# Optimization experiments

Measured on AMD Instinct MI355X. Metric: run time of the kernel, lower is better.

## Reference

```python
import jax, jax.numpy as jnp
import numpy as np

B, T, I, H, O = 256, 256, 16, 256, 11
HYP_HID = 512
BLD = 8
N1 = H * I + H * H + 2 * H        # RNN cell params (W_ih, W_hh, b_ih, b_hh)
N2 = O * H + O                    # readout params (W_out, b_out)


def setup_inputs() -> dict:
    key = jax.random.key(0)
    k = jax.random.split(key, 4)
    bld = jax.random.normal(k[0], (B, BLD), dtype=jnp.float32)
    stimulus = jax.random.normal(k[1], (B, T, I), dtype=jnp.float32)
    # hypnet MLP: bld -> relu -> flat per-sample params; small init to keep tanh unsaturated
    W1 = jax.random.normal(k[2], (BLD, HYP_HID), dtype=jnp.float32) * 0.05
    b1 = jnp.zeros((HYP_HID,), dtype=jnp.float32)
    W2 = jax.random.normal(k[3], (HYP_HID, N1 + N2), dtype=jnp.float32) * 0.02
    b2 = jnp.zeros((N1 + N2,), dtype=jnp.float32)
    return {"bld": bld, "stimulus": stimulus, "W1": W1, "b1": b1, "W2": W2, "b2": b2}


def reference(bld, stimulus, W1, b1, W2, b2):
    # hypernetwork: per-sample flat params [B, N1+N2]
    flat = jax.nn.relu(bld @ W1 + b1) @ W2 + b2
    params1, params2 = flat[:, :N1], flat[:, N1:]

    # unpack per-sample RNN cell params
    o = 0
    W_ih = params1[:, o:o + H * I].reshape(B, H, I); o += H * I
    W_hh = params1[:, o:o + H * H].reshape(B, H, H); o += H * H
    b_ih = params1[:, o:o + H]; o += H
    b_hh = params1[:, o:o + H]
    W_out = params2[:, :O * H].reshape(B, O, H)
    b_out = params2[:, O * H:].reshape(B, O)

    # shift stimulus right by one step with a zero frame (teacher forcing input)
    rnn_input = jnp.concatenate(
        [jnp.zeros((B, 1, I), dtype=stimulus.dtype), stimulus[:, :-1]], axis=1)

    # precompute input projection for all steps: [B, T, H]
    x_proj = jnp.einsum('bti,bhi->bth', rnn_input, W_ih) + b_ih[:, None, :]

    def step(h, xp_t):  # h: [B, H], xp_t: [B, H]
        h_next = jnp.tanh(xp_t + jnp.einsum('bh,bgh->bg', h, W_hh) + b_hh)
        return h_next, h_next

    h0 = jnp.zeros((B, H), dtype=stimulus.dtype)
    h_last, out_tm = jax.lax.scan(step, h0, jnp.swapaxes(x_proj, 0, 1))
    output1 = jnp.swapaxes(out_tm, 0, 1)  # [B, T, H]

    # per-sample linear readout [B, T, O]
    output2 = jnp.einsum('bth,boh->bto', output1, W_out) + b_out[:, None, :]
    output2 = jnp.nan_to_num(output2, nan=0.0)

    output_act = jax.nn.sigmoid(output2[:, :, :3])
    output_bldi = output2[:, :, 3:]
    h = h_last[None]  # [1, B, H]
    return (output_act, output_bldi, h, params1, params2)
```

## Files before the change

kernel.cpp:

```cpp
#include <hip/hip_runtime.h>

typedef unsigned short u16;
typedef unsigned int u32;
using short8   = __attribute__((ext_vector_type(8))) short;
using floatx4  = __attribute__((ext_vector_type(4))) float;
using half_t   = _Float16;
using half2_t  = __attribute__((ext_vector_type(2))) _Float16;
using halfx8   = __attribute__((ext_vector_type(8))) _Float16;

constexpr int B_ = 256, T_ = 256, I_ = 16, H_ = 256, O_ = 11;
constexpr int HYP = 512;
constexpr int N1_ = H_ * I_ + H_ * H_ + 2 * H_;
constexpr int N2_ = O_ * H_ + O_;
constexpr int GN  = N1_ + N2_;

constexpr size_t OUT_ACT  = 0;
constexpr size_t OUT_BLDI = (size_t)B_ * T_ * 3;
constexpr size_t OUT_H    = OUT_BLDI + (size_t)B_ * T_ * 8;
constexpr size_t OUT_P1   = OUT_H + (size_t)B_ * H_;
constexpr size_t OUT_P2   = OUT_P1 + (size_t)B_ * N1_;

__device__ inline void bar_lds() {
    asm volatile("s_waitcnt lgkmcnt(0)\n\ts_barrier" ::: "memory");
}

__device__ inline float bf2f(u16 u) {
    union { u32 i; float f; } v; v.i = ((u32)u) << 16; return v.f;
}
__device__ inline u16 f2bf(float f) {
    u32 x = __float_as_uint(f);
    u32 r = (x + 0x7fffu + ((x >> 16) & 1u)) >> 16;
    return (u16)r;
}

__device__ inline bool sniff_f32(const void* p) {
    const u16* w = (const u16*)p;
    const int lane = threadIdx.x & 63;
    u16 u = w[lane * 2];
    unsigned e = (u >> 7) & 0xFF;
    bool inband = (u == 0) || (e >= 77 && e <= 140);
    return __popcll(__ballot(inband)) < 56;
}

__device__ inline float ldr(const void* p, size_t i, bool f32) {
    return f32 ? ((const float*)p)[i] : bf2f(((const u16*)p)[i]);
}

__global__ void h1_kernel(const void* __restrict__ bld, const void* __restrict__ W1,
                          const void* __restrict__ b1, u16* __restrict__ h1) {
    const bool bldf = sniff_f32(bld);
    const bool w1f  = sniff_f32(W1);
    const bool b1f  = sniff_f32(b1);
    const int b = blockIdx.x;
    const int j = threadIdx.x;
    float acc = ldr(b1, j, b1f);
#pragma unroll
    for (int k = 0; k < 8; k++)
        acc += ldr(bld, b * 8 + k, bldf) * ldr(W1, k * HYP + j, w1f);
    h1[b * HYP + j] = f2bf(fmaxf(acc, 0.f));
}

constexpr int KS_ = 32;
constexpr int NST = HYP / KS_;
constexpr int TKP = 40;

template<bool W2F32>
__device__ void gemm_body(const u16* __restrict__ A, const void* __restrict__ Bm,
                          const void* __restrict__ b2, bool b2f,
                          float* __restrict__ out) {
    __shared__ alignas(16) u16 tileT[2][64][TKP];

    const int nb   = blockIdx.x * 64;
    const int tid  = threadIdx.x;
    const int lane = tid & 63;
    const int wid  = tid >> 6;
    const int l15  = lane & 15;
    const int q    = lane >> 4;

    int  col[4]; bool cv[4];
#pragma unroll
    for (int j = 0; j < 4; j++) {
        int c = nb + j * 16 + l15;
        cv[j]  = (c < GN);
        col[j] = cv[j] ? c : (GN - 1);
    }

    const u16* ap[4];
#pragma unroll
    for (int i = 0; i < 4; i++)
        ap[i] = A + (wid * 64 + i * 16 + l15) * HYP + q * 8;

    const int scol_i = tid & 63;
    const int kq     = tid >> 6;
    int gc = nb + scol_i;
    if (gc >= GN) gc = GN - 1;
    const size_t colOff = (size_t)gc;

    float pfw[8]; u16 pbw[8];
    short8 afc[4];

    {
        float t0[8]; u16 t1[8];
#pragma unroll
        for (int e = 0; e < 8; e++) {
            const size_t ro = (size_t)(kq * 8 + e) * (size_t)GN + colOff;
            if constexpr (W2F32) t0[e] = ((const float*)Bm)[ro];
            else                 t1[e] = ((const u16*)Bm)[ro];
        }
        short8 wv8;
#pragma unroll
        for (int e = 0; e < 8; e++) {
            if constexpr (W2F32) wv8[e] = (short)f2bf(t0[e]);
            else                 wv8[e] = (short)t1[e];
        }
        *(short8*)&tileT[0][scol_i][kq * 8] = wv8;
    }
#pragma unroll
    for (int e = 0; e < 8; e++) {
        const size_t ro = (size_t)(KS_ + kq * 8 + e) * (size_t)GN + colOff;
        if constexpr (W2F32) pfw[e] = ((const float*)Bm)[ro];
        else                 pbw[e] = ((const u16*)Bm)[ro];
    }
#pragma unroll
    for (int i = 0; i < 4; i++) afc[i] = *(const short8*)(ap[i]);
    bar_lds();

    floatx4 acc[4][4] = {};

#pragma unroll
    for (int ks = 0; ks < NST; ks++) {
        const int cur = ks & 1;

        short8 bfr[4];
#pragma unroll
        for (int j = 0; j < 4; j++)
            bfr[j] = *(const short8*)&tileT[cur][j * 16 + l15][q * 8];

        short8 afn[4];
        if (ks + 1 < NST) {
#pragma unroll
            for (int i = 0; i < 4; i++)
                afn[i] = *(const short8*)(ap[i] + (ks + 1) * KS_);
        }
        float pfn[8]; u16 pbn[8];
        if (ks + 2 < NST) {
#pragma unroll
            for (int e = 0; e < 8; e++) {
                const size_t ro = (size_t)((ks + 2) * KS_ + kq * 8 + e) * (size_t)GN + colOff;
                if constexpr (W2F32) pfn[e] = ((const float*)Bm)[ro];
                else                 pbn[e] = ((const u16*)Bm)[ro];
            }
        }
        if (ks + 1 < NST) {
            short8 wv8;
#pragma unroll
            for (int e = 0; e < 8; e++) {
                if constexpr (W2F32) wv8[e] = (short)f2bf(pfw[e]);
                else                 wv8[e] = (short)pbw[e];
            }
            *(short8*)&tileT[cur ^ 1][scol_i][kq * 8] = wv8;
        }

#pragma unroll
        for (int i = 0; i < 4; i++)
#pragma unroll
            for (int j = 0; j < 4; j++)
                acc[i][j] = __builtin_amdgcn_mfma_f32_16x16x32_bf16(afc[i], bfr[j], acc[i][j], 0, 0, 0);
        bar_lds();

#pragma unroll
        for (int i = 0; i < 4; i++) afc[i] = afn[i];
#pragma unroll
        for (int e = 0; e < 8; e++) {
            if constexpr (W2F32) pfw[e] = pfn[e];
            else                 pbw[e] = pbn[e];
        }
    }

    const bool isP2 = (nb >= N1_);
#pragma unroll
    for (int j = 0; j < 4; j++) {
        const float bias = ldr(b2, col[j], b2f);
#pragma unroll
        for (int i = 0; i < 4; i++) {
            const int mbase = wid * 64 + i * 16 + q * 4;
#pragma unroll
            for (int r = 0; r < 4; r++) {
                if (cv[j]) {
                    const float v = acc[i][j][r] + bias;
                    const int m = mbase + r;
                    size_t dst;
                    if (isP2) dst = OUT_P2 + (size_t)m * N2_ + (size_t)(col[j] - N1_);
                    else      dst = OUT_P1 + (size_t)m * N1_ + (size_t)col[j];
                    out[dst] = v;
                }
            }
        }
    }
}
__global__ __launch_bounds__(256) void gemm_kernel(const u16* A, const void* Bm,
                                                   const void* b2, float* out) {
    const bool w2f = sniff_f32(Bm);
    const bool b2f = sniff_f32(b2);
    if (w2f) gemm_body<true>(A, Bm, b2, b2f, out);
    else     gemm_body<false>(A, Bm, b2, b2f, out);
}

constexpr int HROW = 256;
constexpr int XROW = 40;

__global__ __launch_bounds__(512, 1) void rnn_kernel(const void* __restrict__ stim,
                                                     float* __restrict__ out) {
    const bool stf = sniff_f32(stim);
    const int b    = blockIdx.x;
    const int tid  = threadIdx.x;
    const int lane = tid & 63;
    const int wv   = tid >> 6;
    const int l15  = lane & 15;
    const int q    = lane >> 4;

    const float* p1 = out + OUT_P1 + (size_t)b * N1_;
    const float* p2 = out + OUT_P2 + (size_t)b * N2_;

    __shared__ alignas(16) half_t hist[(T_ + 1) * HROW];
    __shared__ alignas(16) half_t stim_s[T_ * XROW];

    if (stf) {
        const float2* sp = (const float2*)stim + (size_t)b * T_ * 8;
        for (int idx = tid; idx < (T_ - 1) * 8; idx += 512) {
            const int tt = idx >> 3, pr = idx & 7;
            float2 v = sp[idx];
            half2_t h; h.x = (half_t)v.x; h.y = (half_t)v.y;
            *(half2_t*)&stim_s[(tt + 1) * XROW + pr * 2] = h;
        }
    } else {
        const u32* sp = (const u32*)((const u16*)stim + (size_t)b * T_ * I_);
        for (int idx = tid; idx < (T_ - 1) * 8; idx += 512) {
            const int tt = idx >> 3, pr = idx & 7;
            u32 u = sp[idx];
            union { u32 i; float f; } lo2, hi2;
            lo2.i = u << 16; hi2.i = u & 0xffff0000u;
            half2_t h; h.x = (half_t)lo2.f; h.y = (half_t)hi2.f;
            *(half2_t*)&stim_s[(tt + 1) * XROW + pr * 2] = h;
        }
    }
    {
        u32* ss = (u32*)stim_s;
        if (tid < 256) {
            const int base = tid * (XROW / 2);
            ss[base + 8] = 0x00003C00u;
#pragma unroll
            for (int z = 9; z < XROW / 2; z++) ss[base + z] = 0u;
        }
        if (tid < 8)   ss[tid] = 0u;
        if (tid < 128) ((u32*)hist)[tid] = 0u;
    }

    halfx8 Wf[2][9];
    {
        const float* WH  = p1 + H_ * I_;
        const float* BIH = p1 + H_ * I_ + H_ * H_;
#pragma unroll
        for (int it = 0; it < 2; it++) {
            const int rr = 32 * wv + it * 16 + l15;
#pragma unroll
            for (int kt = 0; kt < 8; kt++) {
                const float4* wp = (const float4*)(WH + (size_t)rr * H_ + kt * 32 + q * 8);
                float4 r0 = wp[0], r1 = wp[1];
                halfx8 f;
                f[0] = (half_t)r0.x; f[1] = (half_t)r0.y; f[2] = (half_t)r0.z; f[3] = (half_t)r0.w;
                f[4] = (half_t)r1.x; f[5] = (half_t)r1.y; f[6] = (half_t)r1.z; f[7] = (half_t)r1.w;
                Wf[it][kt] = f;
            }
            halfx8 fx;
#pragma unroll
            for (int j = 0; j < 8; j++) fx[j] = (half_t)0.f;
            if (q < 2) {
                const float4* ip = (const float4*)(p1 + (size_t)rr * I_ + q * 8);
                float4 r0 = ip[0], r1 = ip[1];
                fx[0] = (half_t)r0.x; fx[1] = (half_t)r0.y; fx[2] = (half_t)r0.z; fx[3] = (half_t)r0.w;
                fx[4] = (half_t)r1.x; fx[5] = (half_t)r1.y; fx[6] = (half_t)r1.z; fx[7] = (half_t)r1.w;
            } else if (q == 2) {
                fx[0] = (half_t)(BIH[rr] + BIH[H_ + rr]);
            }
            Wf[it][8] = fx;
        }
    }
    __syncthreads();

    for (int t = 0; t < T_; t++) {
        halfx8 af[9];
        const half_t* hr = hist + (size_t)t * HROW + q * 8;
#pragma unroll
        for (int kt = 0; kt < 8; kt++)
            af[kt] = *(const halfx8*)(hr + kt * 32);
        af[8] = *(const halfx8*)(stim_s + (size_t)t * XROW + q * 8);

        floatx4 acc[2] = {};
#pragma unroll
        for (int kt = 0; kt < 9; kt++) {
            acc[0] = __builtin_amdgcn_mfma_f32_16x16x32_f16(af[kt], Wf[0][kt], acc[0], 0, 0, 0);
            acc[1] = __builtin_amdgcn_mfma_f32_16x16x32_f16(af[kt], Wf[1][kt], acc[1], 0, 0, 0);
        }

        half_t* hw = hist + (size_t)(t + 1) * HROW;
#pragma unroll
        for (int it = 0; it < 2; it++) {
            const float s  = acc[it][0];
            const float e  = __expf(2.f * s);
            const float hn = 1.f - 2.f / (e + 1.f);
            if (lane < 16) {
                hw[32 * wv + it * 16 + l15] = (half_t)hn;
                if (t == T_ - 1) out[OUT_H + (size_t)b * H_ + 32 * wv + it * 16 + l15] = hn;
            }
        }
        bar_lds();
    }

    halfx8 Wo[8];
    float bo = 0.f;
    {
#pragma unroll
        for (int kt = 0; kt < 8; kt++) {
            halfx8 f;
#pragma unroll
            for (int j = 0; j < 8; j++) f[j] = (half_t)0.f;
            if (l15 < O_) {
                const float* wp = p2 + (size_t)l15 * H_ + kt * 32 + q * 8;
#pragma unroll
                for (int j = 0; j < 8; j++) f[j] = (half_t)wp[j];
            }
            Wo[kt] = f;
        }
        if (l15 < O_) bo = p2[O_ * H_ + l15];
    }

#pragma unroll
    for (int m = 0; m < 2; m++) {
        const int tb = (2 * wv + m) * 16;
        const half_t* hr = hist + (size_t)(tb + l15 + 1) * HROW + q * 8;
        floatx4 acc = {};
#pragma unroll
        for (int kt = 0; kt < 8; kt++) {
            halfx8 a = *(const halfx8*)(hr + kt * 32);
            acc = __builtin_amdgcn_mfma_f32_16x16x32_f16(a, Wo[kt], acc, 0, 0, 0);
        }
        if (l15 < O_) {
            const int o = l15;
#pragma unroll
            for (int r = 0; r < 4; r++) {
                const int tt = tb + q * 4 + r;
                float v2 = acc[r] + bo;
                if (o < 3) out[OUT_ACT + (size_t)b * T_ * 3 + (size_t)tt * 3 + o] = 1.f / (1.f + __expf(-v2));
                else       out[OUT_BLDI + (size_t)b * T_ * 8 + (size_t)tt * 8 + (o - 3)] = v2;
            }
        }
    }
}

extern "C" void kernel_launch(void* const* d_in, const int* in_sizes, int n_in,
                              void* d_out, int out_size, void* d_ws, size_t ws_size,
                              hipStream_t stream) {
    (void)in_sizes; (void)n_in; (void)out_size; (void)d_ws; (void)ws_size;
    const void* bld  = d_in[0];
    const void* stim = d_in[1];
    const void* W1   = d_in[2];
    const void* b1   = d_in[3];
    const void* W2   = d_in[4];
    const void* b2   = d_in[5];
    float* out = (float*)d_out;
    u16* h1 = (u16*)out;

    h1_kernel<<<B_, HYP, 0, stream>>>(bld, W1, b1, h1);
    gemm_kernel<<<(GN + 63) / 64, 256, 0, stream>>>(h1, W2, b2, out);
    rnn_kernel<<<B_, 512, 0, stream>>>(stim, out);
}
```

Baseline: 437.7 us.

## Precompute input projection for all timesteps before the recurrent loop

Before the time loop, the input projection plus the combined biases is computed for all 256 steps with MFMAs and stored in the hidden-history buffer. That slot is read back each step and overwritten with the new hidden state. This removes one MFMA pair and one LDS load per serial step. The tanh epilogue is also spread across 32 lanes instead of 16 running two passes, and MFMA issue priority is raised with s_setprio. The cost is an extra fp16 rounding of the input projection and an upfront pass over all timesteps.

```diff
diff --git a/kernel.cpp b/kernel.cpp
--- a/kernel.cpp
+++ b/kernel.cpp
@@ -256,7 +256,8 @@
         if (tid < 128) ((u32*)hist)[tid] = 0u;
     }
 
-    halfx8 Wf[2][9];
+    halfx8 Wf[2][8];
+    halfx8 Wx[2];
     {
         const float* WH  = p1 + H_ * I_;
         const float* BIH = p1 + H_ * I_ + H_ * H_;
@@ -283,36 +284,49 @@
             } else if (q == 2) {
                 fx[0] = (half_t)(BIH[rr] + BIH[H_ + rr]);
             }
-            Wf[it][8] = fx;
+            Wx[it] = fx;
         }
     }
     __syncthreads();
 
+#pragma unroll
+    for (int tm = 0; tm < 16; tm++) {
+        halfx8 ax = *(const halfx8*)(stim_s + (size_t)(16 * tm + l15) * XROW + q * 8);
+        floatx4 xa0 = __builtin_amdgcn_mfma_f32_16x16x32_f16(ax, Wx[0], floatx4{}, 0, 0, 0);
+        floatx4 xa1 = __builtin_amdgcn_mfma_f32_16x16x32_f16(ax, Wx[1], floatx4{}, 0, 0, 0);
+#pragma unroll
+        for (int r = 0; r < 4; r++) {
+            const int trow = 16 * tm + 4 * q + r;
+            hist[(size_t)(trow + 1) * HROW + 32 * wv + l15]      = (half_t)xa0[r];
+            hist[(size_t)(trow + 1) * HROW + 32 * wv + 16 + l15] = (half_t)xa1[r];
+        }
+    }
+    __syncthreads();
+
+    const int g32 = 32 * wv + (lane & 31);
     for (int t = 0; t < T_; t++) {
-        halfx8 af[9];
+        halfx8 af[8];
         const half_t* hr = hist + (size_t)t * HROW + q * 8;
 #pragma unroll
         for (int kt = 0; kt < 8; kt++)
             af[kt] = *(const halfx8*)(hr + kt * 32);
-        af[8] = *(const halfx8*)(stim_s + (size_t)t * XROW + q * 8);
-
-        floatx4 acc[2] = {};
-#pragma unroll
-        for (int kt = 0; kt < 9; kt++) {
-            acc[0] = __builtin_amdgcn_mfma_f32_16x16x32_f16(af[kt], Wf[0][kt], acc[0], 0, 0, 0);
-            acc[1] = __builtin_amdgcn_mfma_f32_16x16x32_f16(af[kt], Wf[1][kt], acc[1], 0, 0, 0);
-        }
-
-        half_t* hw = hist + (size_t)(t + 1) * HROW;
-#pragma unroll
-        for (int it = 0; it < 2; it++) {
-            const float s  = acc[it][0];
+        const float xp = (float)hist[(size_t)(t + 1) * HROW + g32];
+
+        floatx4 acc0 = {}, acc1 = {};
+        __builtin_amdgcn_s_setprio(1);
+#pragma unroll
+        for (int kt = 0; kt < 8; kt++) {
+            acc0 = __builtin_amdgcn_mfma_f32_16x16x32_f16(af[kt], Wf[0][kt], acc0, 0, 0, 0);
+            acc1 = __builtin_amdgcn_mfma_f32_16x16x32_f16(af[kt], Wf[1][kt], acc1, 0, 0, 0);
+        }
+        __builtin_amdgcn_s_setprio(0);
+
+        if (lane < 32) {
+            const float s  = ((lane < 16) ? acc0[0] : acc1[0]) + xp;
             const float e  = __expf(2.f * s);
             const float hn = 1.f - 2.f / (e + 1.f);
-            if (lane < 16) {
-                hw[32 * wv + it * 16 + l15] = (half_t)hn;
-                if (t == T_ - 1) out[OUT_H + (size_t)b * H_ + 32 * wv + it * 16 + l15] = hn;
-            }
+            hist[(size_t)(t + 1) * HROW + g32] = (half_t)hn;
+            if (t == T_ - 1) out[OUT_H + (size_t)b * H_ + g32] = hn;
         }
         bar_lds();
     }
```

Result: faster. 417.7 us (-4.6%).
